# Performance work log

Hardware: AMD Instinct MI355X
Metric: run time of the kernel (lower is better)

Reference implementation:

```python
import jax, jax.numpy as jnp
import numpy as np
import math

EMB = 1024
HEADS = 16
B, S = 2, 2048


def setup_inputs() -> dict:
    key = jax.random.key(0)
    k_x, k_wq, k_bq, k_wu, k_bu = jax.random.split(key, 5)
    lim = 1.0 / math.sqrt(EMB)
    x = jax.random.normal(k_x, (B, S, EMB), dtype=jnp.float32)
    # nn.Linear weights: [out, in], uniform(-lim, lim)
    wq = jax.random.uniform(k_wq, (EMB, EMB), jnp.float32, -lim, lim)
    bq = jax.random.uniform(k_bq, (EMB,), jnp.float32, -lim, lim)
    wu = jax.random.uniform(k_wu, (EMB, EMB), jnp.float32, -lim, lim)
    bu = jax.random.uniform(k_bu, (EMB,), jnp.float32, -lim, lim)
    return {"x": x, "wq": wq, "bq": bq, "wu": wu, "bu": bu}


def reference(x, wq, bq, wu, bu):
    b, s, emb = x.shape
    hd = emb // HEADS
    # NOTE: faithful to the original bug — Q, K, V all come from toqueries
    q = jnp.einsum('bse,oe->bso', x, wq) + bq  # [B,S,emb]
    # faithful (buggy) reshape: heads in LEADING dim
    qh = q.reshape(HEADS, b, s, hd)
    kh = qh
    vh = qh
    scale = 1.0 / math.sqrt(emb)  # faithful: sqrt(emb), not sqrt(hd)
    scores = jnp.einsum('hbqd,hbkd->hbqk', qh, kh) * scale  # [H,B,S,S]
    attn = jax.nn.softmax(scores, axis=-1)
    out = jnp.einsum('hbqk,hbkd->hbqd', attn, vh)  # [H,B,S,hd]
    out = out.reshape(b, s, emb)
    return jnp.einsum('bse,oe->bso', out, wu) + bu
```

## Files before the change

### kernel.cpp

```cpp
#include <hip/hip_runtime.h>
#include <stdint.h>

#define EMB 1024
#define HEADS 16
#define NB 2
#define NS 2048
#define HD 64
#define NTOK (NB*NS)
#define KVBLK 64
#define QW 16
#define SEXP2 0.04508421676368185f

typedef __attribute__((ext_vector_type(8))) short short8;
typedef __attribute__((ext_vector_type(4))) float f32x4;
typedef __attribute__((ext_vector_type(4))) unsigned int u32x4;

__device__ inline unsigned short f2bf(float f) {
  unsigned int x = __builtin_bit_cast(unsigned int, f);
  x += 0x7FFFu + ((x >> 16) & 1u);
  return (unsigned short)(x >> 16);
}

__device__ inline unsigned cvt_pk_bf16(float lo, float hi) {
  unsigned d;
  asm("v_cvt_pk_bf16_f32 %0, %1, %2" : "=v"(d) : "v"(lo), "v"(hi));
  return d;
}

__device__ inline void gld16(const void* g, void* l) {
  __builtin_amdgcn_global_load_lds(
      (const __attribute__((address_space(1))) unsigned int*)g,
      (__attribute__((address_space(3))) unsigned int*)l, 16, 0, 0);
}

__global__ void cvt_bf16x3_kernel(const float* __restrict__ s0,
                                  unsigned short* __restrict__ d0, int n0,
                                  const float* __restrict__ s1,
                                  unsigned short* __restrict__ d1, int n1,
                                  const float* __restrict__ s2,
                                  unsigned short* __restrict__ d2, int n2) {
  int i = (blockIdx.x * blockDim.x + threadIdx.x) * 8;
  const float* s; unsigned short* d;
  if (i < n0) { s = s0 + i; d = d0 + i; }
  else if (i - n0 < n1) { s = s1 + (i - n0); d = d1 + (i - n0); }
  else if (i - n0 - n1 < n2) { s = s2 + (i - n0 - n1); d = d2 + (i - n0 - n1); }
  else return;
  float4 v0 = *reinterpret_cast<const float4*>(s);
  float4 v1 = *reinterpret_cast<const float4*>(s + 4);
  short8 o;
  o[0] = (short)f2bf(v0.x); o[1] = (short)f2bf(v0.y);
  o[2] = (short)f2bf(v0.z); o[3] = (short)f2bf(v0.w);
  o[4] = (short)f2bf(v1.x); o[5] = (short)f2bf(v1.y);
  o[6] = (short)f2bf(v1.z); o[7] = (short)f2bf(v1.w);
  *reinterpret_cast<short8*>(d) = o;
}

__global__ __launch_bounds__(256) void transpose_kernel(
    const unsigned short* __restrict__ src, unsigned short* __restrict__ dst) {
  __shared__ unsigned short t[64][72];
  const int slab = blockIdx.y, kt = blockIdx.x;
  const unsigned short* s = src + ((size_t)slab * NS + kt * 64) * HD;
  unsigned short* d = dst + (size_t)slab * HD * NS + kt * 64;
  const int tid = threadIdx.x;
  #pragma unroll
  for (int c = 0; c < 2; ++c) {
    int idx = c * 256 + tid;
    int row = idx >> 3, col = (idx & 7) * 8;
    short8 v = *reinterpret_cast<const short8*>(s + row * HD + col);
    *reinterpret_cast<short8*>(&t[row][col]) = v;
  }
  __syncthreads();
  #pragma unroll
  for (int c = 0; c < 2; ++c) {
    int idx = c * 256 + tid;
    int drow = idx >> 3, col = (idx & 7) * 8;
    short8 v;
    #pragma unroll
    for (int j = 0; j < 8; ++j) {
      int p = col + j;
      int kv = (p & 32) | (((p >> 2) & 1) << 4) | (((p >> 3) & 3) << 2) | (p & 3);
      v[j] = t[kv][drow];
    }
    *reinterpret_cast<short8*>(d + (size_t)drow * NS + col) = v;
  }
}

template<bool OUT_BF16>
__global__ __launch_bounds__(256) void gemm_bt_kernel(
    const unsigned short* __restrict__ A,
    const unsigned short* __restrict__ Bw,
    const float* __restrict__ bias,
    void* __restrict__ Cout,
    unsigned short* __restrict__ Qscaled,
    int M, int N, int K) {
  __shared__ __align__(16) unsigned short As[2][64 * 64];
  __shared__ __align__(16) unsigned short Bs[2][64 * 64];
  const int tid = threadIdx.x;
  const int lane = tid & 63;
  const int wave = tid >> 6;
  const int wr = wave >> 1, wc = wave & 1;
  const int g = lane >> 4, r = lane & 15;
  const int brow = blockIdx.y * 64;
  const int bcol = blockIdx.x * 64;

  const f32x4 zf = {0.f, 0.f, 0.f, 0.f};
  f32x4 acc[2][2];
  #pragma unroll
  for (int m = 0; m < 2; ++m)
    #pragma unroll
    for (int n = 0; n < 2; ++n) acc[m][n] = zf;

  auto stage = [&](int bb, int k0) {
    #pragma unroll
    for (int i = 0; i < 2; ++i) {
      int base = i * 4096 + wave * 1024;
      int L = base + lane * 16;
      int row = L >> 7, lsl = ((L >> 4) & 7) ^ (row & 7);
      gld16((const char*)A + ((size_t)(brow + row) * K + k0) * 2 + lsl * 16,
            (char*)&As[bb][0] + base);
    }
    #pragma unroll
    for (int i = 0; i < 2; ++i) {
      int base = i * 4096 + wave * 1024;
      int L = base + lane * 16;
      int row = L >> 7, lsl = ((L >> 4) & 7) ^ (row & 7);
      gld16((const char*)Bw + ((size_t)(bcol + row) * K + k0) * 2 + lsl * 16,
            (char*)&Bs[bb][0] + base);
    }
  };

  stage(0, 0);
  int cur = 0;
  for (int k0 = 0; k0 < K; k0 += 64) {
    __syncthreads();
    if (k0 + 64 < K) stage(cur ^ 1, k0 + 64);
    const char* Ac = (const char*)&As[cur][0];
    const char* Bc = (const char*)&Bs[cur][0];
    short8 af[2][2], bfr[2][2];
    #pragma unroll
    for (int m = 0; m < 2; ++m) {
      int row = wr * 32 + m * 16 + r;
      #pragma unroll
      for (int kk = 0; kk < 2; ++kk)
        af[m][kk] = *reinterpret_cast<const short8*>(
            Ac + row * 128 + ((kk * 64 + g * 16) ^ ((row & 7) << 4)));
    }
    #pragma unroll
    for (int n = 0; n < 2; ++n) {
      int row = wc * 32 + n * 16 + r;
      #pragma unroll
      for (int kk = 0; kk < 2; ++kk)
        bfr[n][kk] = *reinterpret_cast<const short8*>(
            Bc + row * 128 + ((kk * 64 + g * 16) ^ ((row & 7) << 4)));
    }
    #pragma unroll
    for (int kk = 0; kk < 2; ++kk)
      #pragma unroll
      for (int m = 0; m < 2; ++m)
        #pragma unroll
        for (int n = 0; n < 2; ++n)
          acc[m][n] = __builtin_amdgcn_mfma_f32_16x16x32_bf16(af[m][kk], bfr[n][kk], acc[m][n], 0, 0, 0);
    cur ^= 1;
  }

  #pragma unroll
  for (int n = 0; n < 2; ++n) {
    int col = bcol + wc * 32 + n * 16 + r;
    float bv = bias[col];
    #pragma unroll
    for (int m = 0; m < 2; ++m) {
      #pragma unroll
      for (int reg = 0; reg < 4; ++reg) {
        int row = brow + wr * 32 + m * 16 + g * 4 + reg;
        float v = acc[m][n][reg] + bv;
        if (OUT_BF16)
          ((unsigned short*)Cout)[(size_t)row * N + col] = f2bf(v);
        else
          ((float*)Cout)[(size_t)row * N + col] = v;
        if (Qscaled)
          Qscaled[(size_t)row * N + col] = f2bf(v * SEXP2);
      }
    }
  }
}

__global__ __launch_bounds__(512) void attn_kernel(
    const unsigned short* __restrict__ qb,
    const unsigned short* __restrict__ qsb,
    const unsigned short* __restrict__ vtb,
    unsigned short* __restrict__ ob) {
  const int bid = blockIdx.x;
  const int xcd = bid & 7, idx = bid >> 3;
  const int slab = xcd * 4 + (idx >> 4);
  const int qtile = idx & 15;
  const unsigned short* Qs = qb + (size_t)slab * NS * HD;
  const unsigned short* Qss = qsb + (size_t)slab * NS * HD;
  const unsigned short* Vts = vtb + (size_t)slab * HD * NS;
  unsigned short* Os = ob + (size_t)slab * NS * HD;
  const int tid = threadIdx.x;
  const int lane = tid & 63;
  const int wave = tid >> 6;
  const int g = lane >> 4, r = lane & 15;
  const int qrow0 = qtile * 128 + wave * QW;
  const int rkey = (r & 7) << 4;

  __shared__ __align__(16) unsigned short K_lds[2][KVBLK * HD];
  __shared__ __align__(16) unsigned short Vt_lds[2][HD * KVBLK];

  auto stage = [&](int bb, int kt) {
    const char* Kg = (const char*)(Qs + (size_t)kt * KVBLK * HD);
    const char* Vg = (const char*)Vts + (size_t)kt * 128;
    int base = wave * 1024;
    int L = base + lane * 16;
    int row = L >> 7, lsl = ((L >> 4) & 7) ^ (row & 7);
    gld16(Kg + row * 128 + lsl * 16, (char*)&K_lds[bb][0] + base);
    gld16(Vg + (size_t)row * (NS * 2) + lsl * 16, (char*)&Vt_lds[bb][0] + base);
  };

  short8 aq[2];
  #pragma unroll
  for (int kk = 0; kk < 2; ++kk)
    aq[kk] = *reinterpret_cast<const short8*>(
        &Qss[(size_t)(qrow0 + r) * HD + kk * 32 + g * 8]);

  const f32x4 zf = {0.f, 0.f, 0.f, 0.f};
  f32x4 o_acc[4];
  float l_lane = 0.f;
  #pragma unroll
  for (int n = 0; n < 4; ++n) o_acc[n] = zf;

  stage(0, 0);
  int cur = 0;
  for (int kt = 0; kt < NS / KVBLK; ++kt) {
    __syncthreads();
    if (kt + 1 < NS / KVBLK) stage(cur ^ 1, kt + 1);
    const char* Kc = (const char*)&K_lds[cur][0];
    const char* Vc = (const char*)&Vt_lds[cur][0];

    f32x4 s[4];
    #pragma unroll
    for (int jb = 0; jb < 4; ++jb) {
      short8 bk[2];
      #pragma unroll
      for (int kk = 0; kk < 2; ++kk)
        bk[kk] = *reinterpret_cast<const short8*>(
            Kc + (jb * 16 + r) * 128 + ((kk * 64 + g * 16) ^ rkey));
      s[jb] = zf;
      #pragma unroll
      for (int kk = 0; kk < 2; ++kk)
        s[jb] = __builtin_amdgcn_mfma_f32_16x16x32_bf16(bk[kk], aq[kk], s[jb], 0, 0, 0);
    }

    short8 ap[2];
    {
      float p[4][4];
      #pragma unroll
      for (int jb = 0; jb < 4; ++jb)
        #pragma unroll
        for (int reg = 0; reg < 4; ++reg)
          p[jb][reg] = __builtin_amdgcn_exp2f(s[jb][reg]);
      float t0 = (p[0][0] + p[0][1]) + (p[0][2] + p[0][3]);
      float t1 = (p[1][0] + p[1][1]) + (p[1][2] + p[1][3]);
      float t2 = (p[2][0] + p[2][1]) + (p[2][2] + p[2][3]);
      float t3 = (p[3][0] + p[3][1]) + (p[3][2] + p[3][3]);
      l_lane += (t0 + t1) + (t2 + t3);
      #pragma unroll
      for (int kk = 0; kk < 2; ++kk) {
        u32x4 w;
        w.x = cvt_pk_bf16(p[2 * kk][0], p[2 * kk][1]);
        w.y = cvt_pk_bf16(p[2 * kk][2], p[2 * kk][3]);
        w.z = cvt_pk_bf16(p[2 * kk + 1][0], p[2 * kk + 1][1]);
        w.w = cvt_pk_bf16(p[2 * kk + 1][2], p[2 * kk + 1][3]);
        ap[kk] = __builtin_bit_cast(short8, w);
      }
    }

    #pragma unroll
    for (int n = 0; n < 4; ++n) {
      short8 bv[2];
      #pragma unroll
      for (int kk = 0; kk < 2; ++kk)
        bv[kk] = *reinterpret_cast<const short8*>(
            Vc + (n * 16 + r) * 128 + ((kk * 64 + g * 16) ^ rkey));
      #pragma unroll
      for (int kk = 0; kk < 2; ++kk)
        o_acc[n] = __builtin_amdgcn_mfma_f32_16x16x32_bf16(ap[kk], bv[kk], o_acc[n], 0, 0, 0);
    }
    cur ^= 1;
  }

  {
    float l = l_lane;
    l += __shfl_xor(l, 16);
    l += __shfl_xor(l, 32);
    #pragma unroll
    for (int reg = 0; reg < 4; ++reg) {
      float inv = 1.f / __shfl(l, g * 4 + reg);
      int row = qrow0 + g * 4 + reg;
      #pragma unroll
      for (int n = 0; n < 4; ++n)
        Os[(size_t)row * HD + n * 16 + r] = f2bf(o_acc[n][reg] * inv);
    }
  }
}

extern "C" void kernel_launch(void* const* d_in, const int* in_sizes, int n_in,
                              void* d_out, int out_size, void* d_ws, size_t ws_size,
                              hipStream_t stream) {
  const float* x  = (const float*)d_in[0];
  const float* wq = (const float*)d_in[1];
  const float* bq = (const float*)d_in[2];
  const float* wu = (const float*)d_in[3];
  const float* bu = (const float*)d_in[4];
  float* out = (float*)d_out;

  char* ws = (char*)d_ws;
  unsigned short* xb  = (unsigned short*)(ws);
  unsigned short* qb  = (unsigned short*)(ws + (8u  << 20));
  unsigned short* ob  = (unsigned short*)(ws + (16u << 20));
  unsigned short* wqb = (unsigned short*)(ws + (24u << 20));
  unsigned short* wub = (unsigned short*)(ws + (26u << 20));

  const int nx = NTOK * EMB, nw = EMB * EMB;
  cvt_bf16x3_kernel<<<((nx + 2 * nw) / 8 + 255) / 256, 256, 0, stream>>>(
      x, xb, nx, wq, wqb, nw, wu, wub, nw);

  unsigned short* qsb = ob;
  gemm_bt_kernel<true><<<dim3(EMB / 64, NTOK / 64), 256, 0, stream>>>(
      xb, wqb, bq, qb, qsb, NTOK, EMB, EMB);

  unsigned short* vtb = xb;
  transpose_kernel<<<dim3(NS / 64, HEADS * NB), 256, 0, stream>>>(qb, vtb);

  attn_kernel<<<dim3(512), 512, 0, stream>>>(qb, qsb, vtb, ob);

  gemm_bt_kernel<false><<<dim3(EMB / 64, NTOK / 64), 256, 0, stream>>>(
      ob, wub, bu, out, (unsigned short*)nullptr, NTOK, EMB, EMB);
}
```

Baseline: 91.78 us.

## Double attention KV block to 128 and use 2-wave 64x64 GEMM tiles

The attention kernel now stages 128 keys per iteration instead of 64, processing two 64-key halves per barrier. The V-transpose LDS tile uses a 256-byte row stride with a 16-way XOR swizzle. This halves the number of syncthreads and stage calls and raises LDS use to 64KB. The GEMM kernels go from 4 waves to 2 waves per 64x64 tile, each wave computing a 32x64 strip. That gives more MFMA work per wave but less parallelism per block.

```diff
diff --git a/kernel.cpp b/kernel.cpp
--- a/kernel.cpp
+++ b/kernel.cpp
@@ -7,7 +7,7 @@
 #define NS 2048
 #define HD 64
 #define NTOK (NB*NS)
-#define KVBLK 64
+#define KVBLK 128
 #define QW 16
 #define SEXP2 0.04508421676368185f
 
@@ -86,7 +86,7 @@
 }
 
 template<bool OUT_BF16>
-__global__ __launch_bounds__(256) void gemm_bt_kernel(
+__global__ __launch_bounds__(128) void gemm_bt_kernel(
     const unsigned short* __restrict__ A,
     const unsigned short* __restrict__ Bw,
     const float* __restrict__ bias,
@@ -98,30 +98,29 @@
   const int tid = threadIdx.x;
   const int lane = tid & 63;
   const int wave = tid >> 6;
-  const int wr = wave >> 1, wc = wave & 1;
   const int g = lane >> 4, r = lane & 15;
   const int brow = blockIdx.y * 64;
   const int bcol = blockIdx.x * 64;
 
   const f32x4 zf = {0.f, 0.f, 0.f, 0.f};
-  f32x4 acc[2][2];
+  f32x4 acc[2][4];
   #pragma unroll
   for (int m = 0; m < 2; ++m)
     #pragma unroll
-    for (int n = 0; n < 2; ++n) acc[m][n] = zf;
+    for (int n = 0; n < 4; ++n) acc[m][n] = zf;
 
   auto stage = [&](int bb, int k0) {
     #pragma unroll
-    for (int i = 0; i < 2; ++i) {
-      int base = i * 4096 + wave * 1024;
+    for (int i = 0; i < 4; ++i) {
+      int base = (wave * 4 + i) * 1024;
       int L = base + lane * 16;
       int row = L >> 7, lsl = ((L >> 4) & 7) ^ (row & 7);
       gld16((const char*)A + ((size_t)(brow + row) * K + k0) * 2 + lsl * 16,
             (char*)&As[bb][0] + base);
     }
     #pragma unroll
-    for (int i = 0; i < 2; ++i) {
-      int base = i * 4096 + wave * 1024;
+    for (int i = 0; i < 4; ++i) {
+      int base = (wave * 4 + i) * 1024;
       int L = base + lane * 16;
       int row = L >> 7, lsl = ((L >> 4) & 7) ^ (row & 7);
       gld16((const char*)Bw + ((size_t)(bcol + row) * K + k0) * 2 + lsl * 16,
@@ -136,18 +135,18 @@
     if (k0 + 64 < K) stage(cur ^ 1, k0 + 64);
     const char* Ac = (const char*)&As[cur][0];
     const char* Bc = (const char*)&Bs[cur][0];
-    short8 af[2][2], bfr[2][2];
+    short8 af[2][2], bfr[4][2];
     #pragma unroll
     for (int m = 0; m < 2; ++m) {
-      int row = wr * 32 + m * 16 + r;
+      int row = wave * 32 + m * 16 + r;
       #pragma unroll
       for (int kk = 0; kk < 2; ++kk)
         af[m][kk] = *reinterpret_cast<const short8*>(
             Ac + row * 128 + ((kk * 64 + g * 16) ^ ((row & 7) << 4)));
     }
     #pragma unroll
-    for (int n = 0; n < 2; ++n) {
-      int row = wc * 32 + n * 16 + r;
+    for (int n = 0; n < 4; ++n) {
+      int row = n * 16 + r;
       #pragma unroll
       for (int kk = 0; kk < 2; ++kk)
         bfr[n][kk] = *reinterpret_cast<const short8*>(
@@ -158,20 +157,20 @@
       #pragma unroll
       for (int m = 0; m < 2; ++m)
         #pragma unroll
-        for (int n = 0; n < 2; ++n)
+        for (int n = 0; n < 4; ++n)
           acc[m][n] = __builtin_amdgcn_mfma_f32_16x16x32_bf16(af[m][kk], bfr[n][kk], acc[m][n], 0, 0, 0);
     cur ^= 1;
   }
 
   #pragma unroll
-  for (int n = 0; n < 2; ++n) {
-    int col = bcol + wc * 32 + n * 16 + r;
+  for (int n = 0; n < 4; ++n) {
+    int col = bcol + n * 16 + r;
     float bv = bias[col];
     #pragma unroll
     for (int m = 0; m < 2; ++m) {
       #pragma unroll
       for (int reg = 0; reg < 4; ++reg) {
-        int row = brow + wr * 32 + m * 16 + g * 4 + reg;
+        int row = brow + wave * 32 + m * 16 + g * 4 + reg;
         float v = acc[m][n][reg] + bv;
         if (OUT_BF16)
           ((unsigned short*)Cout)[(size_t)row * N + col] = f2bf(v);
@@ -203,18 +202,23 @@
   const int g = lane >> 4, r = lane & 15;
   const int qrow0 = qtile * 128 + wave * QW;
   const int rkey = (r & 7) << 4;
+  const int vkey = r << 4;
 
   __shared__ __align__(16) unsigned short K_lds[2][KVBLK * HD];
   __shared__ __align__(16) unsigned short Vt_lds[2][HD * KVBLK];
 
   auto stage = [&](int bb, int kt) {
-    const char* Kg = (const char*)(Qs + (size_t)kt * KVBLK * HD);
-    const char* Vg = (const char*)Vts + (size_t)kt * 128;
-    int base = wave * 1024;
-    int L = base + lane * 16;
-    int row = L >> 7, lsl = ((L >> 4) & 7) ^ (row & 7);
-    gld16(Kg + row * 128 + lsl * 16, (char*)&K_lds[bb][0] + base);
-    gld16(Vg + (size_t)row * (NS * 2) + lsl * 16, (char*)&Vt_lds[bb][0] + base);
+    const char* Kg = (const char*)Qs + (size_t)kt * (KVBLK * HD * 2);
+    const char* Vg = (const char*)Vts + (size_t)kt * (KVBLK * 2);
+    #pragma unroll
+    for (int i = 0; i < 2; ++i) {
+      int base = (wave + i * 8) * 1024;
+      int L = base + lane * 16;
+      int krow = L >> 7, klsl = ((L >> 4) & 7) ^ (krow & 7);
+      gld16(Kg + krow * 128 + klsl * 16, (char*)&K_lds[bb][0] + base);
+      int vrow = L >> 8, vlsl = ((L >> 4) & 15) ^ (vrow & 15);
+      gld16(Vg + (size_t)vrow * (NS * 2) + vlsl * 16, (char*)&Vt_lds[bb][0] + base);
+    }
   };
 
   short8 aq[2];
@@ -237,54 +241,57 @@
     const char* Kc = (const char*)&K_lds[cur][0];
     const char* Vc = (const char*)&Vt_lds[cur][0];
 
-    f32x4 s[4];
-    #pragma unroll
-    for (int jb = 0; jb < 4; ++jb) {
-      short8 bk[2];
-      #pragma unroll
-      for (int kk = 0; kk < 2; ++kk)
-        bk[kk] = *reinterpret_cast<const short8*>(
-            Kc + (jb * 16 + r) * 128 + ((kk * 64 + g * 16) ^ rkey));
-      s[jb] = zf;
-      #pragma unroll
-      for (int kk = 0; kk < 2; ++kk)
-        s[jb] = __builtin_amdgcn_mfma_f32_16x16x32_bf16(bk[kk], aq[kk], s[jb], 0, 0, 0);
-    }
-
-    short8 ap[2];
-    {
-      float p[4][4];
-      #pragma unroll
-      for (int jb = 0; jb < 4; ++jb)
-        #pragma unroll
-        for (int reg = 0; reg < 4; ++reg)
-          p[jb][reg] = __builtin_amdgcn_exp2f(s[jb][reg]);
-      float t0 = (p[0][0] + p[0][1]) + (p[0][2] + p[0][3]);
-      float t1 = (p[1][0] + p[1][1]) + (p[1][2] + p[1][3]);
-      float t2 = (p[2][0] + p[2][1]) + (p[2][2] + p[2][3]);
-      float t3 = (p[3][0] + p[3][1]) + (p[3][2] + p[3][3]);
-      l_lane += (t0 + t1) + (t2 + t3);
-      #pragma unroll
-      for (int kk = 0; kk < 2; ++kk) {
-        u32x4 w;
-        w.x = cvt_pk_bf16(p[2 * kk][0], p[2 * kk][1]);
-        w.y = cvt_pk_bf16(p[2 * kk][2], p[2 * kk][3]);
-        w.z = cvt_pk_bf16(p[2 * kk + 1][0], p[2 * kk + 1][1]);
-        w.w = cvt_pk_bf16(p[2 * kk + 1][2], p[2 * kk + 1][3]);
-        ap[kk] = __builtin_bit_cast(short8, w);
+    #pragma unroll
+    for (int h = 0; h < 2; ++h) {
+      f32x4 s[4];
+      #pragma unroll
+      for (int jb = 0; jb < 4; ++jb) {
+        short8 bk[2];
+        #pragma unroll
+        for (int kk = 0; kk < 2; ++kk)
+          bk[kk] = *reinterpret_cast<const short8*>(
+              Kc + (h * 64 + jb * 16 + r) * 128 + ((kk * 64 + g * 16) ^ rkey));
+        s[jb] = zf;
+        #pragma unroll
+        for (int kk = 0; kk < 2; ++kk)
+          s[jb] = __builtin_amdgcn_mfma_f32_16x16x32_bf16(bk[kk], aq[kk], s[jb], 0, 0, 0);
       }
-    }
-
-    #pragma unroll
-    for (int n = 0; n < 4; ++n) {
-      short8 bv[2];
-      #pragma unroll
-      for (int kk = 0; kk < 2; ++kk)
-        bv[kk] = *reinterpret_cast<const short8*>(
-            Vc + (n * 16 + r) * 128 + ((kk * 64 + g * 16) ^ rkey));
-      #pragma unroll
-      for (int kk = 0; kk < 2; ++kk)
-        o_acc[n] = __builtin_amdgcn_mfma_f32_16x16x32_bf16(ap[kk], bv[kk], o_acc[n], 0, 0, 0);
+
+      short8 ap[2];
+      {
+        float p[4][4];
+        #pragma unroll
+        for (int jb = 0; jb < 4; ++jb)
+          #pragma unroll
+          for (int reg = 0; reg < 4; ++reg)
+            p[jb][reg] = __builtin_amdgcn_exp2f(s[jb][reg]);
+        float t0 = (p[0][0] + p[0][1]) + (p[0][2] + p[0][3]);
+        float t1 = (p[1][0] + p[1][1]) + (p[1][2] + p[1][3]);
+        float t2 = (p[2][0] + p[2][1]) + (p[2][2] + p[2][3]);
+        float t3 = (p[3][0] + p[3][1]) + (p[3][2] + p[3][3]);
+        l_lane += (t0 + t1) + (t2 + t3);
+        #pragma unroll
+        for (int kl = 0; kl < 2; ++kl) {
+          u32x4 w;
+          w.x = cvt_pk_bf16(p[2 * kl][0], p[2 * kl][1]);
+          w.y = cvt_pk_bf16(p[2 * kl][2], p[2 * kl][3]);
+          w.z = cvt_pk_bf16(p[2 * kl + 1][0], p[2 * kl + 1][1]);
+          w.w = cvt_pk_bf16(p[2 * kl + 1][2], p[2 * kl + 1][3]);
+          ap[kl] = __builtin_bit_cast(short8, w);
+        }
+      }
+
+      #pragma unroll
+      for (int n = 0; n < 4; ++n) {
+        short8 bv[2];
+        #pragma unroll
+        for (int kl = 0; kl < 2; ++kl)
+          bv[kl] = *reinterpret_cast<const short8*>(
+              Vc + (n * 16 + r) * 256 + (((2 * h + kl) * 64 + g * 16) ^ vkey));
+        #pragma unroll
+        for (int kl = 0; kl < 2; ++kl)
+          o_acc[n] = __builtin_amdgcn_mfma_f32_16x16x32_bf16(ap[kl], bv[kl], o_acc[n], 0, 0, 0);
+      }
     }
     cur ^= 1;
   }
@@ -326,7 +333,7 @@
       x, xb, nx, wq, wqb, nw, wu, wub, nw);
 
   unsigned short* qsb = ob;
-  gemm_bt_kernel<true><<<dim3(EMB / 64, NTOK / 64), 256, 0, stream>>>(
+  gemm_bt_kernel<true><<<dim3(EMB / 64, NTOK / 64), 128, 0, stream>>>(
       xb, wqb, bq, qb, qsb, NTOK, EMB, EMB);
 
   unsigned short* vtb = xb;
@@ -334,6 +341,6 @@
 
   attn_kernel<<<dim3(512), 512, 0, stream>>>(qb, qsb, vtb, ob);
 
-  gemm_bt_kernel<false><<<dim3(EMB / 64, NTOK / 64), 256, 0, stream>>>(
+  gemm_bt_kernel<false><<<dim3(EMB / 64, NTOK / 64), 128, 0, stream>>>(
       ob, wub, bu, out, (unsigned short*)nullptr, NTOK, EMB, EMB);
 }
```

Measured after the change: 103.9 us. +13.2%, slower.
